# Optimization experiments

Measured on AMD Instinct MI355X. Metric: run time of the kernel, lower is better.

## Reference

```python
import jax, jax.numpy as jnp
import numpy as np

DIM = 1024
NUM_HEADS = 16
REL_DIM = 32
B, N = 8, 512


def setup_inputs() -> dict:
    key = jax.random.key(0)
    ks = jax.random.split(key, 8)
    s = 0.02
    return {
        "x": jax.random.normal(ks[0], (B, N, DIM), dtype=jnp.float32),
        "rel_bias": jax.random.normal(ks[1], (B, N, N, REL_DIM), dtype=jnp.float32),
        # torch nn.Linear convention: weight (out_features, in_features)
        "W_qkv": jax.random.normal(ks[2], (3 * DIM, DIM), dtype=jnp.float32) * s,
        "b_qkv": jax.random.normal(ks[3], (3 * DIM,), dtype=jnp.float32) * s,
        "W_rel": jax.random.normal(ks[4], (NUM_HEADS, REL_DIM), dtype=jnp.float32) * s,
        "b_rel": jax.random.normal(ks[5], (NUM_HEADS,), dtype=jnp.float32) * s,
        "W_out": jax.random.normal(ks[6], (DIM, DIM), dtype=jnp.float32) * s,
        "b_out": jax.random.normal(ks[7], (DIM,), dtype=jnp.float32) * s,
    }


def reference(x, rel_bias, W_qkv, b_qkv, W_rel, b_rel, W_out, b_out):
    Bx, Nx, D = x.shape
    H = NUM_HEADS
    hd = D // H
    # QKV projection: (B,N,3D) -> (B,N,3,H,hd)
    qkv = (x @ W_qkv.T + b_qkv).reshape(Bx, Nx, 3, H, hd)
    q, k, v = qkv[:, :, 0], qkv[:, :, 1], qkv[:, :, 2]
    scale = hd ** -0.5
    attn = jnp.einsum('bnhd,bmhd->bhnm', q, k) * scale
    # per-pair relative bias projected to heads: (B,N,N,H) -> (B,H,N,N)
    rel = (rel_bias @ W_rel.T + b_rel).transpose(0, 3, 1, 2)
    attn = jax.nn.softmax(attn + rel, axis=-1)
    out = jnp.einsum('bhnm,bmhd->bnhd', attn, v).reshape(Bx, Nx, D)
    return out @ W_out.T + b_out
```

## Files before the change

kernel.cpp:

```cpp
#include <hip/hip_runtime.h>

typedef unsigned short u16;
typedef unsigned int u32;
typedef __attribute__((ext_vector_type(8))) __bf16 bf16x8;
typedef __attribute__((ext_vector_type(4))) float f32x4;

union U8 {
  bf16x8 b;
  uint2 u2[2];
  uint4 u4;
  u16 us[8];
};

__device__ __forceinline__ u16 f2bf(float f) {
  u32 x = __float_as_uint(f);
  x += 0x7FFFu + ((x >> 16) & 1u);
  return (u16)(x >> 16);
}
__device__ __forceinline__ float bf2f(u16 u) {
  return __uint_as_float(((u32)u) << 16);
}

__global__ void k_convert(const float* __restrict__ src, u16* __restrict__ dst, int n4) {
  int idx = blockIdx.x * blockDim.x + threadIdx.x;
  int stride = gridDim.x * blockDim.x;
  for (int i = idx; i < n4; i += stride) {
    float4 v = ((const float4*)src)[i];
    ushort4 o;
    o.x = f2bf(v.x); o.y = f2bf(v.y); o.z = f2bf(v.z); o.w = f2bf(v.w);
    ((ushort4*)dst)[i] = o;
  }
}

__global__ __launch_bounds__(256) void k_rel(const float* __restrict__ rb,
                                             const float* __restrict__ Wr,
                                             const float* __restrict__ br,
                                             u16* __restrict__ out) {
  __shared__ float Wl[16][32];
  __shared__ float bl[16];
  int t = threadIdx.x;
  ((float*)Wl)[t] = Wr[t];
  ((float*)Wl)[t + 256] = Wr[t + 256];
  if (t < 16) bl[t] = br[t];
  __syncthreads();

  size_t row = (size_t)blockIdx.x * 256 + t;
  int m = (int)(row & 511);
  int n = (int)((row >> 9) & 511);
  int b = (int)(row >> 18);
  const float4* rp = (const float4*)(rb + row * 32);
  float4 r4[8];
#pragma unroll
  for (int j = 0; j < 8; ++j) r4[j] = rp[j];

  size_t obase = (size_t)b * 4194304 + (size_t)n * 512 + m;
#pragma unroll
  for (int h = 0; h < 16; ++h) {
    float acc = bl[h];
    const float* w = Wl[h];
#pragma unroll
    for (int j = 0; j < 8; ++j) {
      acc += r4[j].x * w[4 * j + 0] + r4[j].y * w[4 * j + 1] +
             r4[j].z * w[4 * j + 2] + r4[j].w * w[4 * j + 3];
    }
    out[obase + (size_t)h * 262144] = f2bf(acc);
  }
}

template <int MODE>
__global__ __launch_bounds__(256) void k_gemm(const u16* __restrict__ A,
                                              const u16* __restrict__ Bm,
                                              const float* __restrict__ bias,
                                              u16* __restrict__ Qo, u16* __restrict__ Ko,
                                              u16* __restrict__ Vo, float* __restrict__ Co,
                                              int K) {
  __shared__ u16 Al[128 * 36];
  __shared__ u16 Bl[128 * 36];
  const int t = threadIdx.x;
  const int lane = t & 63, wid = t >> 6;
  const int g = lane >> 4, i16 = lane & 15;
  const int wm = wid >> 1, wn = wid & 1;
  const int bm = blockIdx.y, bn = blockIdx.x;

  f32x4 zero = {0.f, 0.f, 0.f, 0.f};
  f32x4 acc[4][4];
#pragma unroll
  for (int mi = 0; mi < 4; ++mi)
#pragma unroll
    for (int ni = 0; ni < 4; ++ni) acc[mi][ni] = zero;

  const int r0 = t >> 2, c8 = (t & 3) * 8;
  const u16* Ag = A + (size_t)(bm * 128 + r0) * K + c8;
  const u16* Bg = Bm + (size_t)(bn * 128 + r0) * K + c8;

  for (int k0 = 0; k0 < K; k0 += 32) {
    __syncthreads();
    U8 a0, a1, b0, b1;
    a0.u4 = *(const uint4*)(Ag + k0);
    a1.u4 = *(const uint4*)(Ag + k0 + (size_t)64 * K);
    b0.u4 = *(const uint4*)(Bg + k0);
    b1.u4 = *(const uint4*)(Bg + k0 + (size_t)64 * K);
    *(uint2*)(Al + r0 * 36 + c8) = a0.u2[0];
    *(uint2*)(Al + r0 * 36 + c8 + 4) = a0.u2[1];
    *(uint2*)(Al + (r0 + 64) * 36 + c8) = a1.u2[0];
    *(uint2*)(Al + (r0 + 64) * 36 + c8 + 4) = a1.u2[1];
    *(uint2*)(Bl + r0 * 36 + c8) = b0.u2[0];
    *(uint2*)(Bl + r0 * 36 + c8 + 4) = b0.u2[1];
    *(uint2*)(Bl + (r0 + 64) * 36 + c8) = b1.u2[0];
    *(uint2*)(Bl + (r0 + 64) * 36 + c8 + 4) = b1.u2[1];
    __syncthreads();

    U8 af[4], bfg[4];
#pragma unroll
    for (int mi = 0; mi < 4; ++mi) {
      const u16* p = Al + (wm * 64 + mi * 16 + i16) * 36 + 8 * g;
      af[mi].u2[0] = *(const uint2*)p;
      af[mi].u2[1] = *(const uint2*)(p + 4);
    }
#pragma unroll
    for (int ni = 0; ni < 4; ++ni) {
      const u16* p = Bl + (wn * 64 + ni * 16 + i16) * 36 + 8 * g;
      bfg[ni].u2[0] = *(const uint2*)p;
      bfg[ni].u2[1] = *(const uint2*)(p + 4);
    }
#pragma unroll
    for (int mi = 0; mi < 4; ++mi)
#pragma unroll
      for (int ni = 0; ni < 4; ++ni)
        acc[mi][ni] = __builtin_amdgcn_mfma_f32_16x16x32_bf16(af[mi].b, bfg[ni].b,
                                                              acc[mi][ni], 0, 0, 0);
  }

#pragma unroll
  for (int mi = 0; mi < 4; ++mi) {
#pragma unroll
    for (int ni = 0; ni < 4; ++ni) {
      int colb = bn * 128 + wn * 64 + ni * 16;
      int col = colb + i16;
#pragma unroll
      for (int j = 0; j < 4; ++j) {
        int row = bm * 128 + wm * 64 + mi * 16 + 4 * g + j;
        float v = acc[mi][ni][j] + bias[col];
        if (MODE == 0) {
          int tt = col >> 10;
          int h = (col >> 6) & 15;
          int d = col & 63;
          int b = row >> 9;
          int n = row & 511;
          u16* dst = (tt == 0) ? Qo : ((tt == 1) ? Ko : Vo);
          dst[((size_t)(b * 16 + h) * 512 + n) * 64 + d] = f2bf(v);
        } else {
          Co[(size_t)row * 1024 + col] = v;
        }
      }
    }
  }
}

__global__ __launch_bounds__(256) void k_attn(const u16* __restrict__ Q,
                                              const u16* __restrict__ Kb,
                                              const u16* __restrict__ Vb,
                                              const u16* __restrict__ Rel,
                                              u16* __restrict__ Out) {
  __shared__ u16 Kl[64 * 68];
  __shared__ u16 Vt[64 * 68];
  __shared__ u16 Pl[4][16 * 68];

  const int qt = blockIdx.x, h = blockIdx.y, b = blockIdx.z;
  const int t = threadIdx.x, lane = t & 63, wid = t >> 6;
  const int g = lane >> 4, i16 = lane & 15;
  const size_t bh = (size_t)(b * 16 + h);

  const u16* Qg = Q + (bh * 512 + qt * 64 + wid * 16 + i16) * 64;
  U8 qf[2];
  qf[0].u4 = *(const uint4*)(Qg + 8 * g);
  qf[1].u4 = *(const uint4*)(Qg + 8 * g + 32);

  float m_run[4], l_run[4];
  f32x4 zero = {0.f, 0.f, 0.f, 0.f};
  f32x4 acc[4];
#pragma unroll
  for (int c = 0; c < 4; ++c) acc[c] = zero;
#pragma unroll
  for (int j = 0; j < 4; ++j) { m_run[j] = -1e30f; l_run[j] = 0.f; }

  const int r0 = t >> 2, c8 = (t & 3) * 8;
  const u16* Kg = Kb + (bh * 512 + r0) * 64 + c8;
  const u16* Vg = Vb + bh * 512 * 64;
  const u16* Rg = Rel + (bh * 512 + qt * 64 + wid * 16) * 512;

  for (int m0 = 0; m0 < 512; m0 += 64) {
    __syncthreads();
    {
      U8 u0, u1;
      u0.u4 = *(const uint4*)(Kg + m0 * 64);
      u1.u4 = *(const uint4*)(Kg + m0 * 64 + 32);
      *(uint2*)(Kl + r0 * 68 + c8) = u0.u2[0];
      *(uint2*)(Kl + r0 * 68 + c8 + 4) = u0.u2[1];
      *(uint2*)(Kl + r0 * 68 + c8 + 32) = u1.u2[0];
      *(uint2*)(Kl + r0 * 68 + c8 + 36) = u1.u2[1];
    }
    {
      int d = t & 63, mg = t >> 6;
      u16 vr[16];
#pragma unroll
      for (int mm = 0; mm < 16; ++mm)
        vr[mm] = Vg[(size_t)(m0 + mg * 16 + mm) * 64 + d];
#pragma unroll
      for (int jj = 0; jj < 4; ++jj) {
        uint2 w;
        w.x = (u32)vr[4 * jj] | ((u32)vr[4 * jj + 1] << 16);
        w.y = (u32)vr[4 * jj + 2] | ((u32)vr[4 * jj + 3] << 16);
        *(uint2*)(Vt + d * 68 + mg * 16 + 4 * jj) = w;
      }
    }
    __syncthreads();

    f32x4 s[4];
#pragma unroll
    for (int c = 0; c < 4; ++c) s[c] = zero;
#pragma unroll
    for (int c = 0; c < 4; ++c) {
#pragma unroll
      for (int kk = 0; kk < 2; ++kk) {
        U8 kf;
        const u16* p = Kl + (c * 16 + i16) * 68 + 8 * g + 32 * kk;
        kf.u2[0] = *(const uint2*)p;
        kf.u2[1] = *(const uint2*)(p + 4);
        s[c] = __builtin_amdgcn_mfma_f32_16x16x32_bf16(qf[kk].b, kf.b, s[c], 0, 0, 0);
      }
    }
#pragma unroll
    for (int c = 0; c < 4; ++c) {
#pragma unroll
      for (int j = 0; j < 4; ++j) {
        float rv = bf2f(Rg[(size_t)(4 * g + j) * 512 + m0 + c * 16 + i16]);
        s[c][j] = s[c][j] * 0.125f + rv;
      }
    }
    float fac[4];
#pragma unroll
    for (int j = 0; j < 4; ++j) {
      float pm = fmaxf(fmaxf(s[0][j], s[1][j]), fmaxf(s[2][j], s[3][j]));
      pm = fmaxf(pm, __shfl_xor(pm, 1));
      pm = fmaxf(pm, __shfl_xor(pm, 2));
      pm = fmaxf(pm, __shfl_xor(pm, 4));
      pm = fmaxf(pm, __shfl_xor(pm, 8));
      float mnew = fmaxf(m_run[j], pm);
      fac[j] = __expf(m_run[j] - mnew);
      m_run[j] = mnew;
    }
#pragma unroll
    for (int c = 0; c < 4; ++c)
#pragma unroll
      for (int j = 0; j < 4; ++j) s[c][j] = __expf(s[c][j] - m_run[j]);
#pragma unroll
    for (int j = 0; j < 4; ++j) {
      float rs = s[0][j] + s[1][j] + s[2][j] + s[3][j];
      rs += __shfl_xor(rs, 1);
      rs += __shfl_xor(rs, 2);
      rs += __shfl_xor(rs, 4);
      rs += __shfl_xor(rs, 8);
      l_run[j] = l_run[j] * fac[j] + rs;
    }
#pragma unroll
    for (int c = 0; c < 4; ++c)
#pragma unroll
      for (int j = 0; j < 4; ++j) acc[c][j] *= fac[j];

    u16* Pw = Pl[wid];
#pragma unroll
    for (int c = 0; c < 4; ++c)
#pragma unroll
      for (int j = 0; j < 4; ++j)
        Pw[(4 * g + j) * 68 + c * 16 + i16] = f2bf(s[c][j]);
    __syncthreads();

    U8 pf[2];
#pragma unroll
    for (int kk = 0; kk < 2; ++kk) {
      const u16* p = Pl[wid] + i16 * 68 + 8 * g + 32 * kk;
      pf[kk].u2[0] = *(const uint2*)p;
      pf[kk].u2[1] = *(const uint2*)(p + 4);
    }
#pragma unroll
    for (int c = 0; c < 4; ++c) {
#pragma unroll
      for (int kk = 0; kk < 2; ++kk) {
        U8 vf;
        const u16* p = Vt + (c * 16 + i16) * 68 + 8 * g + 32 * kk;
        vf.u2[0] = *(const uint2*)p;
        vf.u2[1] = *(const uint2*)(p + 4);
        acc[c] = __builtin_amdgcn_mfma_f32_16x16x32_bf16(pf[kk].b, vf.b, acc[c], 0, 0, 0);
      }
    }
  }

#pragma unroll
  for (int c = 0; c < 4; ++c) {
#pragma unroll
    for (int j = 0; j < 4; ++j) {
      int n = qt * 64 + wid * 16 + 4 * g + j;
      float v = acc[c][j] / l_run[j];
      Out[((size_t)b * 512 + n) * 1024 + h * 64 + c * 16 + i16] = f2bf(v);
    }
  }
}

extern "C" void kernel_launch(void* const* d_in, const int* in_sizes, int n_in,
                              void* d_out, int out_size, void* d_ws, size_t ws_size,
                              hipStream_t stream) {
  const float* x = (const float*)d_in[0];
  const float* rel_bias = (const float*)d_in[1];
  const float* W_qkv = (const float*)d_in[2];
  const float* b_qkv = (const float*)d_in[3];
  const float* W_rel = (const float*)d_in[4];
  const float* b_rel = (const float*)d_in[5];
  const float* W_out = (const float*)d_in[6];
  const float* b_out = (const float*)d_in[7];
  float* out = (float*)d_out;

  char* ws = (char*)d_ws;
  u16* x_bf    = (u16*)(ws);
  u16* wqkv_bf = (u16*)(ws + 8388608);
  u16* wout_bf = (u16*)(ws + 14680064);
  u16* Qw      = (u16*)(ws + 16777216);
  u16* Kw      = (u16*)(ws + 25165824);
  u16* Vw      = (u16*)(ws + 33554432);
  u16* relb    = (u16*)(ws + 41943040);
  u16* attno   = (u16*)(ws + 109051904);

  k_convert<<<2048, 256, 0, stream>>>(x, x_bf, 4194304 / 4);
  k_convert<<<1024, 256, 0, stream>>>(W_qkv, wqkv_bf, 3145728 / 4);
  k_convert<<<512, 256, 0, stream>>>(W_out, wout_bf, 1048576 / 4);

  k_rel<<<8192, 256, 0, stream>>>(rel_bias, W_rel, b_rel, relb);

  k_gemm<0><<<dim3(24, 32), 256, 0, stream>>>(x_bf, wqkv_bf, b_qkv, Qw, Kw, Vw, nullptr, 1024);

  k_attn<<<dim3(8, 16, 8), 256, 0, stream>>>(Qw, Kw, Vw, relb, attno);

  k_gemm<1><<<dim3(8, 32), 256, 0, stream>>>(attno, wout_bf, b_out, nullptr, nullptr, nullptr,
                                             out, 1024);
}
```

Measured before the change: 212.2 us.

## Use direct global-to-LDS loads with XOR swizzle in GEMM and attention

Replaces register-staged global loads and padded LDS tiles with global_load_lds 16-byte direct transfers into XOR-swizzled LDS in both GEMMs (K step widened from 32 to 64) and in the attention kernel. A separate kernel now pre-transposes V so attention no longer does scalar strided V loads to build the transpose in LDS. This removes VGPR round-trips and bank conflicts on the staging path, at the cost of an extra launch and a V transpose pass that reuses the x_bf workspace.

```diff
diff --git a/kernel.cpp b/kernel.cpp
--- a/kernel.cpp
+++ b/kernel.cpp
@@ -20,6 +20,11 @@
 __device__ __forceinline__ float bf2f(u16 u) {
   return __uint_as_float(((u32)u) << 16);
 }
+
+#define GLOAD16(gp, lp)                                                          \
+  __builtin_amdgcn_global_load_lds(                                              \
+      (const __attribute__((address_space(1))) unsigned int*)(const void*)(gp),  \
+      (__attribute__((address_space(3))) unsigned int*)(void*)(lp), 16, 0, 0)
 
 __global__ void k_convert(const float* __restrict__ src, u16* __restrict__ dst, int n4) {
   int idx = blockIdx.x * blockDim.x + threadIdx.x;
@@ -74,8 +79,8 @@
                                               u16* __restrict__ Qo, u16* __restrict__ Ko,
                                               u16* __restrict__ Vo, float* __restrict__ Co,
                                               int K) {
-  __shared__ u16 Al[128 * 36];
-  __shared__ u16 Bl[128 * 36];
+  __shared__ u16 Al[128 * 64];
+  __shared__ u16 Bl[128 * 64];
   const int t = threadIdx.x;
   const int lane = t & 63, wid = t >> 6;
   const int g = lane >> 4, i16 = lane & 15;
@@ -89,46 +94,50 @@
 #pragma unroll
     for (int ni = 0; ni < 4; ++ni) acc[mi][ni] = zero;
 
-  const int r0 = t >> 2, c8 = (t & 3) * 8;
-  const u16* Ag = A + (size_t)(bm * 128 + r0) * K + c8;
-  const u16* Bg = Bm + (size_t)(bn * 128 + r0) * K + c8;
-
-  for (int k0 = 0; k0 < K; k0 += 32) {
-    __syncthreads();
-    U8 a0, a1, b0, b1;
-    a0.u4 = *(const uint4*)(Ag + k0);
-    a1.u4 = *(const uint4*)(Ag + k0 + (size_t)64 * K);
-    b0.u4 = *(const uint4*)(Bg + k0);
-    b1.u4 = *(const uint4*)(Bg + k0 + (size_t)64 * K);
-    *(uint2*)(Al + r0 * 36 + c8) = a0.u2[0];
-    *(uint2*)(Al + r0 * 36 + c8 + 4) = a0.u2[1];
-    *(uint2*)(Al + (r0 + 64) * 36 + c8) = a1.u2[0];
-    *(uint2*)(Al + (r0 + 64) * 36 + c8 + 4) = a1.u2[1];
-    *(uint2*)(Bl + r0 * 36 + c8) = b0.u2[0];
-    *(uint2*)(Bl + r0 * 36 + c8 + 4) = b0.u2[1];
-    *(uint2*)(Bl + (r0 + 64) * 36 + c8) = b1.u2[0];
-    *(uint2*)(Bl + (r0 + 64) * 36 + c8 + 4) = b1.u2[1];
-    __syncthreads();
-
-    U8 af[4], bfg[4];
-#pragma unroll
-    for (int mi = 0; mi < 4; ++mi) {
-      const u16* p = Al + (wm * 64 + mi * 16 + i16) * 36 + 8 * g;
-      af[mi].u2[0] = *(const uint2*)p;
-      af[mi].u2[1] = *(const uint2*)(p + 4);
-    }
-#pragma unroll
-    for (int ni = 0; ni < 4; ++ni) {
-      const u16* p = Bl + (wn * 64 + ni * 16 + i16) * 36 + 8 * g;
-      bfg[ni].u2[0] = *(const uint2*)p;
-      bfg[ni].u2[1] = *(const uint2*)(p + 4);
-    }
-#pragma unroll
-    for (int mi = 0; mi < 4; ++mi)
-#pragma unroll
-      for (int ni = 0; ni < 4; ++ni)
-        acc[mi][ni] = __builtin_amdgcn_mfma_f32_16x16x32_bf16(af[mi].b, bfg[ni].b,
-                                                              acc[mi][ni], 0, 0, 0);
+  int srow[4], sgc[4];
+#pragma unroll
+  for (int i = 0; i < 4; ++i) {
+    int ch = wid * 256 + i * 64 + lane;
+    int r = ch >> 3, cs = ch & 7;
+    srow[i] = r;
+    sgc[i] = cs ^ (r & 7);
+  }
+
+  for (int k0 = 0; k0 < K; k0 += 64) {
+    __syncthreads();
+#pragma unroll
+    for (int i = 0; i < 4; ++i) {
+      const u16* ga = A + (size_t)(bm * 128 + srow[i]) * K + k0 + sgc[i] * 8;
+      const u16* gb = Bm + (size_t)(bn * 128 + srow[i]) * K + k0 + sgc[i] * 8;
+      u16* la = Al + (size_t)(wid * 256 + i * 64) * 8;
+      u16* lb = Bl + (size_t)(wid * 256 + i * 64) * 8;
+      GLOAD16(ga, la);
+      GLOAD16(gb, lb);
+    }
+    __syncthreads();
+
+#pragma unroll
+    for (int kk = 0; kk < 2; ++kk) {
+      U8 af[4], bfr[4];
+#pragma unroll
+      for (int mi = 0; mi < 4; ++mi) {
+        int row = wm * 64 + mi * 16 + i16;
+        int ch = (g + 4 * kk) ^ (row & 7);
+        af[mi].u4 = *(const uint4*)(Al + row * 64 + ch * 8);
+      }
+#pragma unroll
+      for (int ni = 0; ni < 4; ++ni) {
+        int row = wn * 64 + ni * 16 + i16;
+        int ch = (g + 4 * kk) ^ (row & 7);
+        bfr[ni].u4 = *(const uint4*)(Bl + row * 64 + ch * 8);
+      }
+#pragma unroll
+      for (int mi = 0; mi < 4; ++mi)
+#pragma unroll
+        for (int ni = 0; ni < 4; ++ni)
+          acc[mi][ni] = __builtin_amdgcn_mfma_f32_16x16x32_bf16(af[mi].b, bfr[ni].b,
+                                                                acc[mi][ni], 0, 0, 0);
+    }
   }
 
 #pragma unroll
@@ -157,13 +166,39 @@
   }
 }
 
+__global__ __launch_bounds__(256) void k_vt(const u16* __restrict__ V, u16* __restrict__ Vt) {
+  __shared__ u16 Tl[64][72];
+  const int t = threadIdx.x;
+  const int n0 = blockIdx.x * 64;
+  const size_t bh = blockIdx.y;
+#pragma unroll
+  for (int i = 0; i < 2; ++i) {
+    int c = i * 256 + t;
+    int r = c >> 3, c8 = (c & 7) * 8;
+    U8 v;
+    v.u4 = *(const uint4*)(V + (bh * 512 + n0 + r) * 64 + c8);
+    *(uint2*)&Tl[r][c8] = v.u2[0];
+    *(uint2*)&Tl[r][c8 + 4] = v.u2[1];
+  }
+  __syncthreads();
+#pragma unroll
+  for (int i = 0; i < 2; ++i) {
+    int c = i * 256 + t;
+    int d = c >> 3, n8 = (c & 7) * 8;
+    U8 o;
+#pragma unroll
+    for (int j = 0; j < 8; ++j) o.us[j] = Tl[n8 + j][d];
+    *(uint4*)(Vt + (bh * 64 + d) * 512 + n0 + n8) = o.u4;
+  }
+}
+
 __global__ __launch_bounds__(256) void k_attn(const u16* __restrict__ Q,
                                               const u16* __restrict__ Kb,
-                                              const u16* __restrict__ Vb,
+                                              const u16* __restrict__ Vtb,
                                               const u16* __restrict__ Rel,
                                               u16* __restrict__ Out) {
-  __shared__ u16 Kl[64 * 68];
-  __shared__ u16 Vt[64 * 68];
+  __shared__ u16 Kl[64 * 64];
+  __shared__ u16 Vl[64 * 64];
   __shared__ u16 Pl[4][16 * 68];
 
   const int qt = blockIdx.x, h = blockIdx.y, b = blockIdx.z;
@@ -184,35 +219,27 @@
 #pragma unroll
   for (int j = 0; j < 4; ++j) { m_run[j] = -1e30f; l_run[j] = 0.f; }
 
-  const int r0 = t >> 2, c8 = (t & 3) * 8;
-  const u16* Kg = Kb + (bh * 512 + r0) * 64 + c8;
-  const u16* Vg = Vb + bh * 512 * 64;
+  int srow[2], sgc[2];
+#pragma unroll
+  for (int i = 0; i < 2; ++i) {
+    int ch = wid * 128 + i * 64 + lane;
+    int r = ch >> 3, cs = ch & 7;
+    srow[i] = r;
+    sgc[i] = cs ^ (r & 7);
+  }
+
+  const u16* Kg0 = Kb + bh * 512 * 64;
+  const u16* Vg0 = Vtb + bh * 64 * 512;
   const u16* Rg = Rel + (bh * 512 + qt * 64 + wid * 16) * 512;
 
   for (int m0 = 0; m0 < 512; m0 += 64) {
     __syncthreads();
-    {
-      U8 u0, u1;
-      u0.u4 = *(const uint4*)(Kg + m0 * 64);
-      u1.u4 = *(const uint4*)(Kg + m0 * 64 + 32);
-      *(uint2*)(Kl + r0 * 68 + c8) = u0.u2[0];
-      *(uint2*)(Kl + r0 * 68 + c8 + 4) = u0.u2[1];
-      *(uint2*)(Kl + r0 * 68 + c8 + 32) = u1.u2[0];
-      *(uint2*)(Kl + r0 * 68 + c8 + 36) = u1.u2[1];
-    }
-    {
-      int d = t & 63, mg = t >> 6;
-      u16 vr[16];
-#pragma unroll
-      for (int mm = 0; mm < 16; ++mm)
-        vr[mm] = Vg[(size_t)(m0 + mg * 16 + mm) * 64 + d];
-#pragma unroll
-      for (int jj = 0; jj < 4; ++jj) {
-        uint2 w;
-        w.x = (u32)vr[4 * jj] | ((u32)vr[4 * jj + 1] << 16);
-        w.y = (u32)vr[4 * jj + 2] | ((u32)vr[4 * jj + 3] << 16);
-        *(uint2*)(Vt + d * 68 + mg * 16 + 4 * jj) = w;
-      }
+#pragma unroll
+    for (int i = 0; i < 2; ++i) {
+      u16* lbase = (u16*)0 + (size_t)(wid * 128 + i * 64) * 8;
+      GLOAD16(Kg0 + (size_t)(m0 + srow[i]) * 64 + sgc[i] * 8, Kl + (size_t)(wid * 128 + i * 64) * 8);
+      GLOAD16(Vg0 + (size_t)srow[i] * 512 + m0 + sgc[i] * 8, Vl + (size_t)(wid * 128 + i * 64) * 8);
+      (void)lbase;
     }
     __syncthreads();
 
@@ -223,10 +250,10 @@
     for (int c = 0; c < 4; ++c) {
 #pragma unroll
       for (int kk = 0; kk < 2; ++kk) {
+        int row = c * 16 + i16;
+        int ch = (g + 4 * kk) ^ (row & 7);
         U8 kf;
-        const u16* p = Kl + (c * 16 + i16) * 68 + 8 * g + 32 * kk;
-        kf.u2[0] = *(const uint2*)p;
-        kf.u2[1] = *(const uint2*)(p + 4);
+        kf.u4 = *(const uint4*)(Kl + row * 64 + ch * 8);
         s[c] = __builtin_amdgcn_mfma_f32_16x16x32_bf16(qf[kk].b, kf.b, s[c], 0, 0, 0);
       }
     }
@@ -287,10 +314,10 @@
     for (int c = 0; c < 4; ++c) {
 #pragma unroll
       for (int kk = 0; kk < 2; ++kk) {
+        int row = c * 16 + i16;
+        int ch = (g + 4 * kk) ^ (row & 7);
         U8 vf;
-        const u16* p = Vt + (c * 16 + i16) * 68 + 8 * g + 32 * kk;
-        vf.u2[0] = *(const uint2*)p;
-        vf.u2[1] = *(const uint2*)(p + 4);
+        vf.u4 = *(const uint4*)(Vl + row * 64 + ch * 8);
         acc[c] = __builtin_amdgcn_mfma_f32_16x16x32_bf16(pf[kk].b, vf.b, acc[c], 0, 0, 0);
       }
     }
@@ -322,6 +349,7 @@
 
   char* ws = (char*)d_ws;
   u16* x_bf    = (u16*)(ws);
+  u16* Vt      = (u16*)(ws);
   u16* wqkv_bf = (u16*)(ws + 8388608);
   u16* wout_bf = (u16*)(ws + 14680064);
   u16* Qw      = (u16*)(ws + 16777216);
@@ -338,7 +366,9 @@
 
   k_gemm<0><<<dim3(24, 32), 256, 0, stream>>>(x_bf, wqkv_bf, b_qkv, Qw, Kw, Vw, nullptr, 1024);
 
-  k_attn<<<dim3(8, 16, 8), 256, 0, stream>>>(Qw, Kw, Vw, relb, attno);
+  k_vt<<<dim3(8, 128), 256, 0, stream>>>(Vw, Vt);
+
+  k_attn<<<dim3(8, 16, 8), 256, 0, stream>>>(Qw, Kw, Vt, relb, attno);
 
   k_gemm<1><<<dim3(8, 32), 256, 0, stream>>>(attno, wout_bf, b_out, nullptr, nullptr, nullptr,
                                              out, 1024);
```

Result: faster. 200.4 us (-5.6%).
